# Kernel optimization log

Hardware: AMD Instinct MI355X
Metric: run time of the kernel (lower is better)

## Reference

```python
import jax, jax.numpy as jnp
import numpy as np

B, L, H = 8, 512, 768
W = 5          # max_phrase_len
K = 32         # max_phrases
P = 256        # phrase_dim
EPS = 1e-5
NEG = -1e30


def layernorm(x, g, b):
    m = jnp.mean(x, axis=-1, keepdims=True)
    v = jnp.var(x, axis=-1, keepdims=True)
    return (x - m) * jax.lax.rsqrt(v + EPS) * g + b


def setup_inputs() -> dict:
    key = jax.random.key(0)
    ks = jax.random.split(key, 12)
    s = 0.02
    return {
        "hidden": jax.random.normal(ks[0], (B, L, H), dtype=jnp.float32),
        "attention_mask": jnp.ones((B, L), dtype=jnp.int32),
        # span_scorer: Linear(4H->H), LayerNorm(H), ReLU, Linear(H->1)
        "w1": jax.random.normal(ks[1], (4 * H, H), dtype=jnp.float32) * s,
        "b1": jnp.zeros((H,), dtype=jnp.float32),
        "g1": jnp.ones((H,), dtype=jnp.float32),
        "beta1": jnp.zeros((H,), dtype=jnp.float32),
        "w2": jax.random.normal(ks[2], (H, 1), dtype=jnp.float32) * s,
        "b2": jnp.zeros((1,), dtype=jnp.float32),
        # proj: Linear(H->P)
        "wp": jax.random.normal(ks[3], (H, P), dtype=jnp.float32) * s,
        "bp": jnp.zeros((P,), dtype=jnp.float32),
        # attention_gate: Linear(H->H/2), Tanh, Linear(H/2->1)
        "wg1": jax.random.normal(ks[4], (H, H // 2), dtype=jnp.float32) * s,
        "bg1": jnp.zeros((H // 2,), dtype=jnp.float32),
        "wg2": jax.random.normal(ks[5], (H // 2, 1), dtype=jnp.float32) * s,
        "bg2": jnp.zeros((1,), dtype=jnp.float32),
        # out_norm: LayerNorm(P)
        "gout": jnp.ones((P,), dtype=jnp.float32),
        "bout": jnp.zeros((P,), dtype=jnp.float32),
    }


def reference(hidden, attention_mask, w1, b1, g1, beta1, w2, b2,
              wp, bp, wg1, bg1, wg2, bg2, gout, bout):
    mask = attention_mask.astype(bool)  # [B,L]
    # validity of span (i, j=i+w): all tokens i..i+w in mask and i+w < L
    valids = []
    v = mask
    for w in range(W):
        if w > 0:
            shifted = jnp.pad(mask[:, w:], ((0, 0), (0, w)), constant_values=False)
            v = v & shifted
        valids.append(v)
    valid = jnp.stack(valids, axis=2)  # [B,L,W]

    # span means via prefix sums
    prefix = jnp.pad(jnp.cumsum(hidden, axis=1), ((0, 0), (1, 0), (0, 0)))  # [B,L+1,H]
    i_idx = jnp.arange(L)
    j_idx = jnp.minimum(i_idx[:, None] + jnp.arange(W)[None, :], L - 1)  # [L,W]

    start = hidden[:, :, None, :]                                  # [B,L,1,H]
    end = hidden[:, j_idx]                                         # [B,L,W,H]
    span_sum = prefix[:, j_idx + 1] - prefix[:, i_idx][:, :, None, :]
    mean = span_sum / (jnp.arange(W, dtype=hidden.dtype) + 1.0)[None, None, :, None]
    diff = end - start
    start_b = jnp.broadcast_to(start, end.shape)
    feat = jnp.concatenate([start_b, end, mean, diff], axis=-1)    # [B,L,W,4H]

    h = feat @ w1 + b1
    h = jax.nn.relu(layernorm(h, g1, beta1))                       # dropout is eval-mode identity
    score = (h @ w2 + b2)[..., 0]                                  # [B,L,W]
    score = jnp.where(valid, score, NEG)

    flat_scores = score.reshape(B, L * W)
    top_scores, top_idx = jax.lax.top_k(flat_scores, K)            # [B,K]
    phrase_masks = top_scores > NEG / 2

    mean_flat = mean.reshape(B, L * W, H)
    embs = jnp.take_along_axis(mean_flat, top_idx[..., None], axis=1)  # [B,K,H]
    embs = jnp.where(phrase_masks[..., None], embs, 0.0)               # zero-pad features
    phrase_scores = jnp.where(phrase_masks, top_scores, -10.0)

    ti = top_idx // W
    tw = top_idx % W
    spans = jnp.stack([ti, ti + tw], axis=-1)                      # [B,K,2]
    spans = jnp.where(phrase_masks[..., None], spans, 0)

    gate_logits = (jnp.tanh(embs @ wg1 + bg1) @ wg2 + bg2)[..., 0]  # [B,K]
    gate_logits = jnp.where(phrase_masks, gate_logits, -1e9)
    phrase_attention = jax.nn.softmax(gate_logits, axis=-1)

    phrase_embeds = layernorm(embs @ wp + bp, gout, bout)           # [B,K,P]
    return phrase_embeds, phrase_masks, phrase_attention, phrase_scores, spans
```

## Files before the change

kernel.cpp:

```cpp
#include <hip/hip_runtime.h>
#include <float.h>
#include <math.h>

#define B_   8
#define L_   512
#define H_   768
#define W_   5
#define K_   32
#define P_   256
#define EPS_ 1e-5f
#define NEG_ -1e30f

typedef _Float16 half8 __attribute__((ext_vector_type(8)));
typedef _Float16 half4v __attribute__((ext_vector_type(4)));
typedef float floatx4 __attribute__((ext_vector_type(4)));

static const size_t OFF_X   = 0;
static const size_t OFF_AH  = 9437184;
static const size_t OFF_AL  = 11010048;
static const size_t OFF_BH  = 12582912;
static const size_t OFF_BL  = 13467648;
static const size_t OFF_SC  = 14352384;
static const size_t OFF_TS  = 14372864;
static const size_t OFF_TI  = 14373120;
static const size_t OFF_GL  = 14373376;
static const size_t OFF_EMB = 14373632;
static const size_t OFF_Y   = 14570240;

#define A_SCALE 8.0f
#define B_SCALE 64.0f
#define INV_SCALE (1.0f / 512.0f)

__global__ __launch_bounds__(256) void split_hidden_kernel(const float* __restrict__ hid,
                                                           _Float16* __restrict__ ah,
                                                           _Float16* __restrict__ al) {
    int idx = (blockIdx.x * 256 + threadIdx.x) * 4;
    float4 x = *(const float4*)(hid + idx);
    float xs[4] = {x.x * A_SCALE, x.y * A_SCALE, x.z * A_SCALE, x.w * A_SCALE};
    half4v h, l;
#pragma unroll
    for (int i = 0; i < 4; ++i) {
        _Float16 hi = (_Float16)xs[i];
        h[i] = hi;
        l[i] = (_Float16)(xs[i] - (float)hi);
    }
    *(half4v*)(ah + idx) = h;
    *(half4v*)(al + idx) = l;
}

__global__ __launch_bounds__(256) void build_wt_kernel(const float* __restrict__ w1,
                                                       _Float16* __restrict__ bh,
                                                       _Float16* __restrict__ bl) {
    __shared__ float ld[64][65];
    int n0 = blockIdx.x * 64;
    int k0 = blockIdx.y * 64;
    int t = threadIdx.x;
    int rsel = n0 / 768;
    int c0 = n0 - rsel * 768;
#pragma unroll 4
    for (int r = 0; r < 16; ++r) {
        int idx = r * 256 + t;
        int kk = idx >> 6, nn = idx & 63;
        int k = k0 + kk, c = c0 + nn;
        float v;
        if (rsel == 0)      v = w1[(size_t)k * 768 + c] - w1[(size_t)(2304 + k) * 768 + c];
        else if (rsel == 1) v = w1[(size_t)(768 + k) * 768 + c] + w1[(size_t)(2304 + k) * 768 + c];
        else                v = w1[(size_t)(1536 + k) * 768 + c];
        ld[kk][nn] = v * B_SCALE;
    }
    __syncthreads();
#pragma unroll 4
    for (int r = 0; r < 16; ++r) {
        int idx = r * 256 + t;
        int nn = idx >> 6, kk = idx & 63;
        float v = ld[kk][nn];
        _Float16 h = (_Float16)v;
        _Float16 lo = (_Float16)(v - (float)h);
        size_t o = (size_t)(n0 + nn) * 768 + k0 + kk;
        bh[o] = h;
        bl[o] = lo;
    }
}

typedef const __attribute__((address_space(1))) void* gas_ptr;
typedef __attribute__((address_space(3))) void* las_ptr;
__device__ __forceinline__ void async_ld16(const _Float16* g, _Float16* l) {
    __builtin_amdgcn_global_load_lds((gas_ptr)g, (las_ptr)l, 16, 0, 0);
}

__global__ __launch_bounds__(256) void mfma_gemm_kernel(const _Float16* __restrict__ Ah,
                                                        const _Float16* __restrict__ Al,
                                                        const _Float16* __restrict__ Bh,
                                                        const _Float16* __restrict__ Bl,
                                                        float* __restrict__ C) {
    __shared__ _Float16 sAh[128 * 32];
    __shared__ _Float16 sAl[128 * 32];
    __shared__ _Float16 sBh[128 * 32];
    __shared__ _Float16 sBl[128 * 32];
    int tid = threadIdx.x;
    int lane = tid & 63;
    int wave = tid >> 6;
    int m0 = blockIdx.x * 128, n0 = blockIdx.y * 128;

    const _Float16* src = (wave == 0) ? Ah : (wave == 1) ? Al : (wave == 2) ? Bh : Bl;
    _Float16* dst = (wave == 0) ? sAh : (wave == 1) ? sAl : (wave == 2) ? sBh : sBl;
    int row0 = (wave < 2) ? m0 : n0;
    int qg = (lane & 3) ^ ((lane >> 3) & 3);
    const _Float16* gp = src + (size_t)(row0 + (lane >> 2)) * 768 + qg * 8;

    int wr = wave >> 1, wc = wave & 1;
    int off_lane = (lane & 15) * 64 + (((lane >> 4) ^ ((lane >> 1) & 3)) * 16);
    const char* pAh = (const char*)sAh + wr * 4096 + off_lane;
    const char* pAl = (const char*)sAl + wr * 4096 + off_lane;
    const char* pBh = (const char*)sBh + wc * 4096 + off_lane;
    const char* pBl = (const char*)sBl + wc * 4096 + off_lane;

    floatx4 acc[4][4];
#pragma unroll
    for (int i = 0; i < 4; ++i)
#pragma unroll
        for (int j = 0; j < 4; ++j)
            acc[i][j] = (floatx4){0.f, 0.f, 0.f, 0.f};

    for (int k0 = 0; k0 < 768; k0 += 32) {
        __syncthreads();
#pragma unroll
        for (int c = 0; c < 8; ++c)
            async_ld16(gp + k0 + (size_t)c * 16 * 768, dst + c * 512);
        __syncthreads();

        half8 a_h[4], a_l[4], b_h[4], b_l[4];
#pragma unroll
        for (int i = 0; i < 4; ++i) {
            a_h[i] = *(const half8*)(pAh + i * 1024);
            a_l[i] = *(const half8*)(pAl + i * 1024);
            b_h[i] = *(const half8*)(pBh + i * 1024);
            b_l[i] = *(const half8*)(pBl + i * 1024);
        }
#pragma unroll
        for (int i = 0; i < 4; ++i)
#pragma unroll
            for (int j = 0; j < 4; ++j) {
                acc[i][j] = __builtin_amdgcn_mfma_f32_16x16x32_f16(a_h[i], b_h[j], acc[i][j], 0, 0, 0);
                acc[i][j] = __builtin_amdgcn_mfma_f32_16x16x32_f16(a_h[i], b_l[j], acc[i][j], 0, 0, 0);
                acc[i][j] = __builtin_amdgcn_mfma_f32_16x16x32_f16(a_l[i], b_h[j], acc[i][j], 0, 0, 0);
            }
    }

    int colc = lane & 15, quad = lane >> 4;
#pragma unroll
    for (int i = 0; i < 4; ++i) {
#pragma unroll
        for (int r = 0; r < 4; ++r) {
            int row = m0 + wr * 64 + i * 16 + quad * 4 + r;
            float* Cp = C + (size_t)row * 2304 + n0 + wc * 64 + colc;
#pragma unroll
            for (int j = 0; j < 4; ++j)
                Cp[j * 16] = acc[i][j][r] * INV_SCALE;
        }
    }
}

__global__ __launch_bounds__(256) void score_kernel(const float* __restrict__ X,
                                                    const int* __restrict__ mask,
                                                    const float* __restrict__ b1,
                                                    const float* __restrict__ g1,
                                                    const float* __restrict__ beta1,
                                                    const float* __restrict__ w2,
                                                    const float* __restrict__ b2,
                                                    float* __restrict__ scores) {
    int wave = threadIdx.x >> 6;
    int lane = threadIdx.x & 63;
    int bi = blockIdx.x * 4 + wave;
    int b = bi >> 9, i = bi & 511;

    float a[12], b1c[12], g1c[12], btc[12], w2c[12], ss[12], e[12];
    const float* Xrow = X + (size_t)bi * 2304;
#pragma unroll
    for (int q = 0; q < 12; ++q) {
        int c = lane + q * 64;
        a[q]   = Xrow[c];
        b1c[q] = b1[c];
        g1c[q] = g1[c];
        btc[q] = beta1[c];
        w2c[q] = w2[c];
        ss[q]  = 0.f;
    }
    float bias2 = b2[0];
    int jcur = i - 1;
    float sc_loc[W_];

    for (int w = 0; w < W_; ++w) {
        int j = min(i + w, 511);
        const float* Xj = X + (size_t)(b * 512 + j) * 2304;
        if (j > jcur) {
#pragma unroll
            for (int q = 0; q < 12; ++q) {
                int c = lane + q * 64;
                ss[q] += Xj[1536 + c];
                e[q]   = Xj[768 + c];
            }
            jcur = j;
        }
        float invw = 1.0f / (float)(w + 1);
        float h[12];
        float psum = 0.f;
#pragma unroll
        for (int q = 0; q < 12; ++q) {
            h[q] = a[q] + e[q] + ss[q] * invw + b1c[q];
            psum += h[q];
        }
#pragma unroll
        for (int m = 1; m < 64; m <<= 1) psum += __shfl_xor(psum, m, 64);
        float mean = psum * (1.f / 768.f);

        float pv = 0.f;
#pragma unroll
        for (int q = 0; q < 12; ++q) {
            float d = h[q] - mean;
            pv += d * d;
        }
#pragma unroll
        for (int m = 1; m < 64; m <<= 1) pv += __shfl_xor(pv, m, 64);
        float rstd = rsqrtf(pv * (1.f / 768.f) + EPS_);

        float pd = 0.f;
#pragma unroll
        for (int q = 0; q < 12; ++q) {
            float d = h[q] - mean;
            float y = fmaxf(d * rstd * g1c[q] + btc[q], 0.f);
            pd += y * w2c[q];
        }
#pragma unroll
        for (int m = 1; m < 64; m <<= 1) pd += __shfl_xor(pd, m, 64);
        sc_loc[w] = pd + bias2;
    }

    if (lane < W_) {
        int w = lane;
        bool ok = (i + w) < 512;
        if (ok) {
            for (int t = 0; t <= w; ++t) ok = ok && (mask[b * 512 + i + t] != 0);
        }
        scores[b * 2560 + i * 5 + w] = ok ? sc_loc[w] : NEG_;
    }
}

__global__ __launch_bounds__(256) void topk_kernel(const float* __restrict__ scores,
                                                   float* __restrict__ tops,
                                                   int* __restrict__ topi,
                                                   float* __restrict__ out_masks,
                                                   float* __restrict__ out_scores,
                                                   float* __restrict__ out_spans) {
    int b = blockIdx.x;
    int tid = threadIdx.x;
    int lane = tid & 63;
    int wv = tid >> 6;
    __shared__ float sc[2560];
    __shared__ float wv_v[4];
    __shared__ int   wv_i[4];
    for (int t = tid; t < 2560; t += 256) sc[t] = scores[b * 2560 + t];
    __syncthreads();

    for (int k = 0; k < K_; ++k) {
        float bv = -FLT_MAX; int bix = 1 << 30;
        for (int t = tid; t < 2560; t += 256) {
            float v = sc[t];
            if (v > bv || (v == bv && t < bix)) { bv = v; bix = t; }
        }
#pragma unroll
        for (int m = 1; m < 64; m <<= 1) {
            float v2 = __shfl_xor(bv, m, 64);
            int   i2 = __shfl_xor(bix, m, 64);
            if (v2 > bv || (v2 == bv && i2 < bix)) { bv = v2; bix = i2; }
        }
        if (lane == 0) { wv_v[wv] = bv; wv_i[wv] = bix; }
        __syncthreads();
        if (tid == 0) {
            float tv = wv_v[0]; int tix = wv_i[0];
            for (int q = 1; q < 4; ++q) {
                if (wv_v[q] > tv || (wv_v[q] == tv && wv_i[q] < tix)) { tv = wv_v[q]; tix = wv_i[q]; }
            }
            tops[b * 32 + k] = tv;
            topi[b * 32 + k] = tix;
            bool m = tv > (NEG_ * 0.5f);
            out_masks[b * 32 + k] = m ? 1.0f : 0.0f;
            out_scores[b * 32 + k] = m ? tv : -10.0f;
            int tI = tix / 5, tw = tix % 5;
            out_spans[(b * 32 + k) * 2 + 0] = m ? (float)tI : 0.0f;
            out_spans[(b * 32 + k) * 2 + 1] = m ? (float)(tI + tw) : 0.0f;
            sc[tix] = -FLT_MAX;
        }
        __syncthreads();
    }
}

__global__ __launch_bounds__(256) void gather_emb_kernel(const float* __restrict__ hidden,
                                                         const float* __restrict__ tops,
                                                         const int* __restrict__ topi,
                                                         float* __restrict__ Embs) {
    int bk = blockIdx.x;
    int b = bk >> 5;
    int tid = threadIdx.x;
    int idx = topi[bk];
    bool valid = tops[bk] > (NEG_ * 0.5f);
    int tI = idx / 5, tw = idx % 5;
    int jend = min(tI + tw, L_ - 1);
    float inv = 1.0f / (float)(tw + 1);
#pragma unroll
    for (int q = 0; q < 3; ++q) {
        int c = tid + q * 256;
        float s = 0.f;
        if (valid) {
            for (int l = tI; l <= jend; ++l) s += hidden[(size_t)(b * 512 + l) * 768 + c];
            s *= inv;
        }
        Embs[(size_t)bk * 768 + c] = s;
    }
}

__global__ __launch_bounds__(256) void phrase_gemm_kernel(const float* __restrict__ Embs,
                                                          const float* __restrict__ wg1,
                                                          const float* __restrict__ bg1,
                                                          const float* __restrict__ wp,
                                                          const float* __restrict__ bp,
                                                          float* __restrict__ Y) {
    __shared__ float As[32][34];
    __shared__ float Bs[32][64];
    int tid = threadIdx.x;
    int m0 = blockIdx.x * 32;
    int cn0 = blockIdx.y * 64;
    const float* Wp; const float* biasp; int ldw;
    if (cn0 < 384) { Wp = wg1 + cn0;        biasp = bg1 + cn0;        ldw = 384; }
    else           { Wp = wp + (cn0 - 384); biasp = bp + (cn0 - 384); ldw = 256; }

    int tx = tid & 15;
    int ty = tid >> 4;
    int ar = tid >> 3, akq = (tid & 7) * 4;
    int bk = tid >> 3, bcq = (tid & 7) * 8;
    float acc[2][4] = {};

    for (int k0 = 0; k0 < 768; k0 += 32) {
        float4 av  = *(const float4*)(Embs + (size_t)(m0 + ar) * 768 + k0 + akq);
        float4 bv0 = *(const float4*)(Wp + (size_t)(k0 + bk) * ldw + bcq);
        float4 bv1 = *(const float4*)(Wp + (size_t)(k0 + bk) * ldw + bcq + 4);
        __syncthreads();
        As[akq + 0][ar] = av.x;
        As[akq + 1][ar] = av.y;
        As[akq + 2][ar] = av.z;
        As[akq + 3][ar] = av.w;
        *(float4*)&Bs[bk][bcq]     = bv0;
        *(float4*)&Bs[bk][bcq + 4] = bv1;
        __syncthreads();
#pragma unroll
        for (int kk = 0; kk < 32; ++kk) {
            float2 a = *(const float2*)&As[kk][ty * 2];
            float4 b = *(const float4*)&Bs[kk][tx * 4];
            acc[0][0] += a.x * b.x; acc[0][1] += a.x * b.y; acc[0][2] += a.x * b.z; acc[0][3] += a.x * b.w;
            acc[1][0] += a.y * b.x; acc[1][1] += a.y * b.y; acc[1][2] += a.y * b.z; acc[1][3] += a.y * b.w;
        }
    }
#pragma unroll
    for (int i = 0; i < 2; ++i) {
        float* Yp = Y + (size_t)(m0 + ty * 2 + i) * 640 + cn0 + tx * 4;
        float4 o = make_float4(acc[i][0] + biasp[tx * 4 + 0], acc[i][1] + biasp[tx * 4 + 1],
                               acc[i][2] + biasp[tx * 4 + 2], acc[i][3] + biasp[tx * 4 + 3]);
        *(float4*)Yp = o;
    }
}

__global__ __launch_bounds__(256) void phrase_post_kernel(const float* __restrict__ Y,
                                                          const float* __restrict__ wg2,
                                                          const float* __restrict__ bg2,
                                                          const float* __restrict__ tops,
                                                          const float* __restrict__ gout,
                                                          const float* __restrict__ bout,
                                                          float* __restrict__ gate,
                                                          float* __restrict__ out_embeds) {
    int wv = threadIdx.x >> 6, lane = threadIdx.x & 63;
    int row = blockIdx.x * 4 + wv;
    const float* Yrow = Y + (size_t)row * 640;

    float s = 0.f;
#pragma unroll
    for (int q = 0; q < 6; ++q) {
        int c = lane + q * 64;
        s += tanhf(Yrow[c]) * wg2[c];
    }
#pragma unroll
    for (int m = 1; m < 64; m <<= 1) s += __shfl_xor(s, m, 64);
    if (lane == 0) {
        bool valid = tops[row] > (NEG_ * 0.5f);
        gate[row] = valid ? (s + bg2[0]) : -1e9f;
    }

    float4 p = *(const float4*)(Yrow + 384 + lane * 4);
    float sm = p.x + p.y + p.z + p.w;
#pragma unroll
    for (int m = 1; m < 64; m <<= 1) sm += __shfl_xor(sm, m, 64);
    float mean = sm * (1.f / 256.f);
    float dx = p.x - mean, dy = p.y - mean, dz = p.z - mean, dw = p.w - mean;
    float v = dx * dx + dy * dy + dz * dz + dw * dw;
#pragma unroll
    for (int m = 1; m < 64; m <<= 1) v += __shfl_xor(v, m, 64);
    float rstd = rsqrtf(v * (1.f / 256.f) + EPS_);
    int c = lane * 4;
    float4 o;
    o.x = dx * rstd * gout[c]     + bout[c];
    o.y = dy * rstd * gout[c + 1] + bout[c + 1];
    o.z = dz * rstd * gout[c + 2] + bout[c + 2];
    o.w = dw * rstd * gout[c + 3] + bout[c + 3];
    *(float4*)(out_embeds + (size_t)row * 256 + c) = o;
}

__global__ void attn_kernel(const float* __restrict__ gate, float* __restrict__ out_attn) {
    int b = threadIdx.x;
    if (b < 8) {
        float mx = -FLT_MAX;
        for (int k = 0; k < 32; ++k) mx = fmaxf(mx, gate[b * 32 + k]);
        float e[32];
        float s = 0.f;
        for (int k = 0; k < 32; ++k) { e[k] = expf(gate[b * 32 + k] - mx); s += e[k]; }
        float inv = 1.f / s;
        for (int k = 0; k < 32; ++k) out_attn[b * 32 + k] = e[k] * inv;
    }
}

extern "C" void kernel_launch(void* const* d_in, const int* in_sizes, int n_in,
                              void* d_out, int out_size, void* d_ws, size_t ws_size,
                              hipStream_t stream) {
    const float* hidden = (const float*)d_in[0];
    const int*   amask  = (const int*)d_in[1];
    const float* w1     = (const float*)d_in[2];
    const float* b1     = (const float*)d_in[3];
    const float* g1     = (const float*)d_in[4];
    const float* beta1  = (const float*)d_in[5];
    const float* w2     = (const float*)d_in[6];
    const float* b2     = (const float*)d_in[7];
    const float* wp     = (const float*)d_in[8];
    const float* bp     = (const float*)d_in[9];
    const float* wg1    = (const float*)d_in[10];
    const float* bg1    = (const float*)d_in[11];
    const float* wg2    = (const float*)d_in[12];
    const float* bg2    = (const float*)d_in[13];
    const float* gout   = (const float*)d_in[14];
    const float* bout   = (const float*)d_in[15];

    float* ws = (float*)d_ws;
    float*     X    = ws + OFF_X;
    _Float16*  ah   = (_Float16*)(ws + OFF_AH);
    _Float16*  al   = (_Float16*)(ws + OFF_AL);
    _Float16*  bh   = (_Float16*)(ws + OFF_BH);
    _Float16*  bl   = (_Float16*)(ws + OFF_BL);
    float*     sc   = ws + OFF_SC;
    float*     ts   = ws + OFF_TS;
    int*       ti   = (int*)(ws + OFF_TI);
    float*     gl   = ws + OFF_GL;
    float*     Embs = ws + OFF_EMB;
    float*     Y    = ws + OFF_Y;

    float* out = (float*)d_out;
    float* out_embeds = out;
    float* out_masks  = out + 65536;
    float* out_attn   = out + 65792;
    float* out_scores = out + 66048;
    float* out_spans  = out + 66304;

    split_hidden_kernel<<<3072, 256, 0, stream>>>(hidden, ah, al);
    build_wt_kernel<<<dim3(36, 12), 256, 0, stream>>>(w1, bh, bl);
    mfma_gemm_kernel<<<dim3(32, 18), 256, 0, stream>>>(ah, al, bh, bl, X);
    score_kernel<<<1024, 256, 0, stream>>>(X, amask, b1, g1, beta1, w2, b2, sc);
    topk_kernel<<<8, 256, 0, stream>>>(sc, ts, ti, out_masks, out_scores, out_spans);
    gather_emb_kernel<<<256, 256, 0, stream>>>(hidden, ts, ti, Embs);
    phrase_gemm_kernel<<<dim3(8, 10), 256, 0, stream>>>(Embs, wg1, bg1, wp, bp, Y);
    phrase_post_kernel<<<64, 256, 0, stream>>>(Y, wg2, bg2, ts, gout, bout, gl, out_embeds);
    attn_kernel<<<1, 64, 0, stream>>>(gl, out_attn);
}
```

Before: 286.3 us.

## Double-buffer GEMM LDS tiles, halve N tile, merge prep kernels, vectorize score loads

```diff
diff --git a/kernel.cpp b/kernel.cpp
--- a/kernel.cpp
+++ b/kernel.cpp
@@ -31,54 +31,56 @@
 #define B_SCALE 64.0f
 #define INV_SCALE (1.0f / 512.0f)
 
-__global__ __launch_bounds__(256) void split_hidden_kernel(const float* __restrict__ hid,
-                                                           _Float16* __restrict__ ah,
-                                                           _Float16* __restrict__ al) {
-    int idx = (blockIdx.x * 256 + threadIdx.x) * 4;
-    float4 x = *(const float4*)(hid + idx);
-    float xs[4] = {x.x * A_SCALE, x.y * A_SCALE, x.z * A_SCALE, x.w * A_SCALE};
-    half4v h, l;
-#pragma unroll
-    for (int i = 0; i < 4; ++i) {
-        _Float16 hi = (_Float16)xs[i];
-        h[i] = hi;
-        l[i] = (_Float16)(xs[i] - (float)hi);
-    }
-    *(half4v*)(ah + idx) = h;
-    *(half4v*)(al + idx) = l;
-}
-
-__global__ __launch_bounds__(256) void build_wt_kernel(const float* __restrict__ w1,
-                                                       _Float16* __restrict__ bh,
-                                                       _Float16* __restrict__ bl) {
+__global__ __launch_bounds__(256) void prep_kernel(const float* __restrict__ hid,
+                                                   const float* __restrict__ w1,
+                                                   _Float16* __restrict__ ah,
+                                                   _Float16* __restrict__ al,
+                                                   _Float16* __restrict__ bh,
+                                                   _Float16* __restrict__ bl) {
     __shared__ float ld[64][65];
-    int n0 = blockIdx.x * 64;
-    int k0 = blockIdx.y * 64;
-    int t = threadIdx.x;
-    int rsel = n0 / 768;
-    int c0 = n0 - rsel * 768;
+    if (blockIdx.x < 3072) {
+        int idx = (blockIdx.x * 256 + threadIdx.x) * 4;
+        float4 x = *(const float4*)(hid + idx);
+        float xs[4] = {x.x * A_SCALE, x.y * A_SCALE, x.z * A_SCALE, x.w * A_SCALE};
+        half4v h, l;
+#pragma unroll
+        for (int i = 0; i < 4; ++i) {
+            _Float16 hi = (_Float16)xs[i];
+            h[i] = hi;
+            l[i] = (_Float16)(xs[i] - (float)hi);
+        }
+        *(half4v*)(ah + idx) = h;
+        *(half4v*)(al + idx) = l;
+    } else {
+        int bid = blockIdx.x - 3072;
+        int n0 = (bid / 12) * 64;
+        int k0 = (bid % 12) * 64;
+        int t = threadIdx.x;
+        int rsel = n0 / 768;
+        int c0 = n0 - rsel * 768;
 #pragma unroll 4
-    for (int r = 0; r < 16; ++r) {
-        int idx = r * 256 + t;
-        int kk = idx >> 6, nn = idx & 63;
-        int k = k0 + kk, c = c0 + nn;
-        float v;
-        if (rsel == 0)      v = w1[(size_t)k * 768 + c] - w1[(size_t)(2304 + k) * 768 + c];
-        else if (rsel == 1) v = w1[(size_t)(768 + k) * 768 + c] + w1[(size_t)(2304 + k) * 768 + c];
-        else                v = w1[(size_t)(1536 + k) * 768 + c];
-        ld[kk][nn] = v * B_SCALE;
-    }
-    __syncthreads();
+        for (int r = 0; r < 16; ++r) {
+            int idx = r * 256 + t;
+            int kk = idx >> 6, nn = idx & 63;
+            int k = k0 + kk, c = c0 + nn;
+            float v;
+            if (rsel == 0)      v = w1[(size_t)k * 768 + c] - w1[(size_t)(2304 + k) * 768 + c];
+            else if (rsel == 1) v = w1[(size_t)(768 + k) * 768 + c] + w1[(size_t)(2304 + k) * 768 + c];
+            else                v = w1[(size_t)(1536 + k) * 768 + c];
+            ld[kk][nn] = v * B_SCALE;
+        }
+        __syncthreads();
 #pragma unroll 4
-    for (int r = 0; r < 16; ++r) {
-        int idx = r * 256 + t;
-        int nn = idx >> 6, kk = idx & 63;
-        float v = ld[kk][nn];
-        _Float16 h = (_Float16)v;
-        _Float16 lo = (_Float16)(v - (float)h);
-        size_t o = (size_t)(n0 + nn) * 768 + k0 + kk;
-        bh[o] = h;
-        bl[o] = lo;
+        for (int r = 0; r < 16; ++r) {
+            int idx = r * 256 + t;
+            int nn = idx >> 6, kk = idx & 63;
+            float v = ld[kk][nn];
+            _Float16 h = (_Float16)v;
+            _Float16 lo = (_Float16)(v - (float)h);
+            size_t o = (size_t)(n0 + nn) * 768 + k0 + kk;
+            bh[o] = h;
+            bl[o] = lo;
+        }
     }
 }
 
@@ -93,58 +95,73 @@
                                                         const _Float16* __restrict__ Bh,
                                                         const _Float16* __restrict__ Bl,
                                                         float* __restrict__ C) {
-    __shared__ _Float16 sAh[128 * 32];
-    __shared__ _Float16 sAl[128 * 32];
-    __shared__ _Float16 sBh[128 * 32];
-    __shared__ _Float16 sBl[128 * 32];
+    __shared__ _Float16 sAh[2 * 4096];
+    __shared__ _Float16 sAl[2 * 4096];
+    __shared__ _Float16 sBh[2 * 2048];
+    __shared__ _Float16 sBl[2 * 2048];
     int tid = threadIdx.x;
     int lane = tid & 63;
     int wave = tid >> 6;
-    int m0 = blockIdx.x * 128, n0 = blockIdx.y * 128;
+    int m0 = blockIdx.x * 128, n0 = blockIdx.y * 64;
 
     const _Float16* src = (wave == 0) ? Ah : (wave == 1) ? Al : (wave == 2) ? Bh : Bl;
-    _Float16* dst = (wave == 0) ? sAh : (wave == 1) ? sAl : (wave == 2) ? sBh : sBl;
+    _Float16* dstb = (wave == 0) ? sAh : (wave == 1) ? sAl : (wave == 2) ? sBh : sBl;
+    int psz  = (wave < 2) ? 4096 : 2048;
+    int nch  = (wave < 2) ? 8 : 4;
     int row0 = (wave < 2) ? m0 : n0;
     int qg = (lane & 3) ^ ((lane >> 3) & 3);
     const _Float16* gp = src + (size_t)(row0 + (lane >> 2)) * 768 + qg * 8;
 
     int wr = wave >> 1, wc = wave & 1;
     int off_lane = (lane & 15) * 64 + (((lane >> 4) ^ ((lane >> 1) & 3)) * 16);
-    const char* pAh = (const char*)sAh + wr * 4096 + off_lane;
-    const char* pAl = (const char*)sAl + wr * 4096 + off_lane;
-    const char* pBh = (const char*)sBh + wc * 4096 + off_lane;
-    const char* pBl = (const char*)sBl + wc * 4096 + off_lane;
-
-    floatx4 acc[4][4];
+    floatx4 acc[4][2];
 #pragma unroll
     for (int i = 0; i < 4; ++i)
 #pragma unroll
-        for (int j = 0; j < 4; ++j)
+        for (int j = 0; j < 2; ++j)
             acc[i][j] = (floatx4){0.f, 0.f, 0.f, 0.f};
 
+#pragma unroll
+    for (int c = 0; c < 8; ++c) {
+        if (c < nch) async_ld16(gp + (size_t)c * 16 * 768, dstb + c * 512);
+    }
+
+    int parity = 0;
     for (int k0 = 0; k0 < 768; k0 += 32) {
         __syncthreads();
-#pragma unroll
-        for (int c = 0; c < 8; ++c)
-            async_ld16(gp + k0 + (size_t)c * 16 * 768, dst + c * 512);
-        __syncthreads();
-
-        half8 a_h[4], a_l[4], b_h[4], b_l[4];
+        if (k0 + 32 < 768) {
+            _Float16* dst = dstb + (parity ^ 1) * psz;
+            const _Float16* g = gp + k0 + 32;
+#pragma unroll
+            for (int c = 0; c < 8; ++c) {
+                if (c < nch) async_ld16(g + (size_t)c * 16 * 768, dst + c * 512);
+            }
+        }
+
+        const char* bAh = (const char*)sAh + parity * 8192 + wr * 4096 + off_lane;
+        const char* bAl = (const char*)sAl + parity * 8192 + wr * 4096 + off_lane;
+        const char* bBh = (const char*)sBh + parity * 4096 + wc * 2048 + off_lane;
+        const char* bBl = (const char*)sBl + parity * 4096 + wc * 2048 + off_lane;
+        half8 a_h[4], a_l[4], b_h[2], b_l[2];
 #pragma unroll
         for (int i = 0; i < 4; ++i) {
-            a_h[i] = *(const half8*)(pAh + i * 1024);
-            a_l[i] = *(const half8*)(pAl + i * 1024);
-            b_h[i] = *(const half8*)(pBh + i * 1024);
-            b_l[i] = *(const half8*)(pBl + i * 1024);
+            a_h[i] = *(const half8*)(bAh + i * 1024);
+            a_l[i] = *(const half8*)(bAl + i * 1024);
+        }
+#pragma unroll
+        for (int j = 0; j < 2; ++j) {
+            b_h[j] = *(const half8*)(bBh + j * 1024);
+            b_l[j] = *(const half8*)(bBl + j * 1024);
         }
 #pragma unroll
         for (int i = 0; i < 4; ++i)
 #pragma unroll
-            for (int j = 0; j < 4; ++j) {
+            for (int j = 0; j < 2; ++j) {
                 acc[i][j] = __builtin_amdgcn_mfma_f32_16x16x32_f16(a_h[i], b_h[j], acc[i][j], 0, 0, 0);
                 acc[i][j] = __builtin_amdgcn_mfma_f32_16x16x32_f16(a_h[i], b_l[j], acc[i][j], 0, 0, 0);
                 acc[i][j] = __builtin_amdgcn_mfma_f32_16x16x32_f16(a_l[i], b_h[j], acc[i][j], 0, 0, 0);
             }
+        parity ^= 1;
     }
 
     int colc = lane & 15, quad = lane >> 4;
@@ -153,9 +170,9 @@
 #pragma unroll
         for (int r = 0; r < 4; ++r) {
             int row = m0 + wr * 64 + i * 16 + quad * 4 + r;
-            float* Cp = C + (size_t)row * 2304 + n0 + wc * 64 + colc;
-#pragma unroll
-            for (int j = 0; j < 4; ++j)
+            float* Cp = C + (size_t)row * 2304 + n0 + wc * 32 + colc;
+#pragma unroll
+            for (int j = 0; j < 2; ++j)
                 Cp[j * 16] = acc[i][j][r] * INV_SCALE;
         }
     }
@@ -174,17 +191,17 @@
     int bi = blockIdx.x * 4 + wave;
     int b = bi >> 9, i = bi & 511;
 
-    float a[12], b1c[12], g1c[12], btc[12], w2c[12], ss[12], e[12];
-    const float* Xrow = X + (size_t)bi * 2304;
-#pragma unroll
-    for (int q = 0; q < 12; ++q) {
-        int c = lane + q * 64;
-        a[q]   = Xrow[c];
-        b1c[q] = b1[c];
-        g1c[q] = g1[c];
-        btc[q] = beta1[c];
-        w2c[q] = w2[c];
-        ss[q]  = 0.f;
+    float4 a[3], b1c[3], g1c[3], btc[3], w2c[3], ss[3], e[3];
+    const float4* Xrow = (const float4*)(X + (size_t)bi * 2304);
+#pragma unroll
+    for (int q = 0; q < 3; ++q) {
+        int f = lane + q * 64;
+        a[q]   = Xrow[f];
+        b1c[q] = ((const float4*)b1)[f];
+        g1c[q] = ((const float4*)g1)[f];
+        btc[q] = ((const float4*)beta1)[f];
+        w2c[q] = ((const float4*)w2)[f];
+        ss[q]  = make_float4(0.f, 0.f, 0.f, 0.f);
     }
     float bias2 = b2[0];
     int jcur = i - 1;
@@ -192,23 +209,27 @@
 
     for (int w = 0; w < W_; ++w) {
         int j = min(i + w, 511);
-        const float* Xj = X + (size_t)(b * 512 + j) * 2304;
+        const float4* Xj = (const float4*)(X + (size_t)(b * 512 + j) * 2304);
         if (j > jcur) {
 #pragma unroll
-            for (int q = 0; q < 12; ++q) {
-                int c = lane + q * 64;
-                ss[q] += Xj[1536 + c];
-                e[q]   = Xj[768 + c];
+            for (int q = 0; q < 3; ++q) {
+                int f = lane + q * 64;
+                float4 cc = Xj[384 + f];
+                ss[q].x += cc.x; ss[q].y += cc.y; ss[q].z += cc.z; ss[q].w += cc.w;
+                e[q] = Xj[192 + f];
             }
             jcur = j;
         }
         float invw = 1.0f / (float)(w + 1);
-        float h[12];
+        float4 h[3];
         float psum = 0.f;
 #pragma unroll
-        for (int q = 0; q < 12; ++q) {
-            h[q] = a[q] + e[q] + ss[q] * invw + b1c[q];
-            psum += h[q];
+        for (int q = 0; q < 3; ++q) {
+            h[q].x = a[q].x + e[q].x + ss[q].x * invw + b1c[q].x;
+            h[q].y = a[q].y + e[q].y + ss[q].y * invw + b1c[q].y;
+            h[q].z = a[q].z + e[q].z + ss[q].z * invw + b1c[q].z;
+            h[q].w = a[q].w + e[q].w + ss[q].w * invw + b1c[q].w;
+            psum += h[q].x + h[q].y + h[q].z + h[q].w;
         }
 #pragma unroll
         for (int m = 1; m < 64; m <<= 1) psum += __shfl_xor(psum, m, 64);
@@ -216,9 +237,9 @@
 
         float pv = 0.f;
 #pragma unroll
-        for (int q = 0; q < 12; ++q) {
-            float d = h[q] - mean;
-            pv += d * d;
+        for (int q = 0; q < 3; ++q) {
+            float dx = h[q].x - mean, dy = h[q].y - mean, dz = h[q].z - mean, dw = h[q].w - mean;
+            pv += dx * dx + dy * dy + dz * dz + dw * dw;
         }
 #pragma unroll
         for (int m = 1; m < 64; m <<= 1) pv += __shfl_xor(pv, m, 64);
@@ -226,10 +247,12 @@
 
         float pd = 0.f;
 #pragma unroll
-        for (int q = 0; q < 12; ++q) {
-            float d = h[q] - mean;
-            float y = fmaxf(d * rstd * g1c[q] + btc[q], 0.f);
-            pd += y * w2c[q];
+        for (int q = 0; q < 3; ++q) {
+            float yx = fmaxf((h[q].x - mean) * rstd * g1c[q].x + btc[q].x, 0.f);
+            float yy = fmaxf((h[q].y - mean) * rstd * g1c[q].y + btc[q].y, 0.f);
+            float yz = fmaxf((h[q].z - mean) * rstd * g1c[q].z + btc[q].z, 0.f);
+            float yw = fmaxf((h[q].w - mean) * rstd * g1c[q].w + btc[q].w, 0.f);
+            pd += yx * w2c[q].x + yy * w2c[q].y + yz * w2c[q].z + yw * w2c[q].w;
         }
 #pragma unroll
         for (int m = 1; m < 64; m <<= 1) pd += __shfl_xor(pd, m, 64);
@@ -466,9 +489,8 @@
     float* out_scores = out + 66048;
     float* out_spans  = out + 66304;
 
-    split_hidden_kernel<<<3072, 256, 0, stream>>>(hidden, ah, al);
-    build_wt_kernel<<<dim3(36, 12), 256, 0, stream>>>(w1, bh, bl);
-    mfma_gemm_kernel<<<dim3(32, 18), 256, 0, stream>>>(ah, al, bh, bl, X);
+    prep_kernel<<<3504, 256, 0, stream>>>(hidden, w1, ah, al, bh, bl);
+    mfma_gemm_kernel<<<dim3(32, 36), 256, 0, stream>>>(ah, al, bh, bl, X);
     score_kernel<<<1024, 256, 0, stream>>>(X, amask, b1, g1, beta1, w2, b2, sc);
     topk_kernel<<<8, 256, 0, stream>>>(sc, ts, ti, out_masks, out_scores, out_spans);
     gather_emb_kernel<<<256, 256, 0, stream>>>(hidden, ts, ti, Embs);
```

Result: faster. 276.3 us (-3.5%).
